# Optimization experiments

Measured on AMD Instinct MI355X. Metric: run time of the kernel, lower is better.

Reference implementation:

```python
import jax, jax.numpy as jnp
import numpy as np

N = 50000   # total nodes (50 graphs x 1000 nodes)
E = 800000  # edges (avg degree 16)
H = 128     # hidden_dim == input_dim
B = 50      # number of graphs
L = 3       # n_GNN_layers
NEG = 0.2   # LeakyReLU slope
EPS = 1e-5  # BatchNorm eps


def _lrelu(v):
    return jnp.where(v >= 0, v, NEG * v)


def setup_inputs() -> dict:
    key = jax.random.key(0)
    ks = jax.random.split(key, 16)
    s = 0.05
    inp = {
        "x": jax.random.normal(ks[0], (N, H), jnp.float32),
        "edge_index": jax.random.randint(ks[1], (2, E), 0, N, dtype=jnp.int64),
        "edge_attr": jax.random.uniform(ks[2], (E,), jnp.float32),
        "batch": jnp.sort(jax.random.randint(ks[3], (N,), 0, B, dtype=jnp.int64)),
        # per-layer GCN params (3 identical-shape layers stacked on axis 0)
        "Wg": (jax.random.normal(ks[4], (L, H, H)) * s).astype(jnp.float32),   # GCNConv.lin (no bias)
        "bg": jnp.zeros((L, H), jnp.float32),                                  # GCNConv.bias
        "We": (jax.random.normal(ks[5], (L, 2 * H, H)) * s).astype(jnp.float32),  # edge_lin
        "be": jnp.zeros((L, H), jnp.float32),
        "Wl": (jax.random.normal(ks[6], (L, H, H)) * s).astype(jnp.float32),   # post-conv Linear
        "bl": jnp.zeros((L, H), jnp.float32),
        "gamma": jnp.ones((L, H), jnp.float32),                                # BatchNorm affine
        "beta": jnp.zeros((L, H), jnp.float32),
        # final MLP head
        "Wf1": (jax.random.normal(ks[7], (H, H)) * s).astype(jnp.float32),
        "bf1": jnp.zeros((H,), jnp.float32),
        "Wf2": (jax.random.normal(ks[8], (H, H // 2)) * s).astype(jnp.float32),
        "bf2": jnp.zeros((H // 2,), jnp.float32),
        "Wf3": (jax.random.normal(ks[9], (H // 2, 2)) * s).astype(jnp.float32),
        "bf3": jnp.zeros((2,), jnp.float32),
    }
    return inp


def reference(x, edge_index, edge_attr, batch, Wg, bg, We, be, Wl, bl, gamma, beta,
              Wf1, bf1, Wf2, bf2, Wf3, bf3):
    n = x.shape[0]
    # edge_attr = |edge_attr| is used only for gcn_norm's edge weights, which the
    # 'node_concate' message ignores; self-loops from gcn_norm DO affect messages.
    _ = jnp.abs(edge_attr)
    loop = jnp.arange(n, dtype=edge_index.dtype)
    row = jnp.concatenate([edge_index[0], loop])  # source j
    col = jnp.concatenate([edge_index[1], loop])  # target i

    z = x
    for l in range(L):
        h = z @ Wg[l]                                           # GCNConv.lin (bias=False)
        msg = jnp.concatenate([h[col], h[row]], axis=1) @ We[l] + be[l]  # edge_lin(cat[x_i, x_j])
        agg = jax.ops.segment_sum(msg, col, num_segments=n) + bg[l]      # scatter-add + conv bias
        h2 = _lrelu(agg @ Wl[l] + bl[l])                        # Linear + LeakyReLU(0.2)
        mu = h2.mean(axis=0)
        var = h2.var(axis=0)                                    # biased var (BatchNorm training)
        z = gamma[l] * (h2 - mu) * jax.lax.rsqrt(var + EPS) + beta[l]

    # global_mean_pool over graph segments
    sums = jax.ops.segment_sum(z, batch, num_segments=B)
    cnt = jax.ops.segment_sum(jnp.ones((n, 1), z.dtype), batch, num_segments=B)
    pooled = sums / jnp.maximum(cnt, 1.0)

    h = _lrelu(pooled @ Wf1 + bf1)
    h = _lrelu(h @ Wf2 + bf2)
    return h @ Wf3 + bf3
```

## Files before the change

### kernel.cpp

```cpp
#include <hip/hip_runtime.h>
#include <hip/hip_fp16.h>

#define H 128
#define NEG 0.2f
#define EPSBN 1e-5f
#define BM 32

__device__ __forceinline__ float lrelu(float v){ return v >= 0.f ? v : NEG*v; }

union HU { __half2 h; unsigned int u; };

typedef __attribute__((ext_vector_type(8))) short bf16x8;
typedef __attribute__((ext_vector_type(4))) float f32x4;
#define MFMA16(a,b,c) __builtin_amdgcn_mfma_f32_16x16x32_bf16(a,b,c,0,0,0)

__device__ __forceinline__ unsigned short bf16_rn(float x){
  unsigned int u = __float_as_uint(x);
  u += 0x7fffu + ((u >> 16) & 1u);
  return (unsigned short)(u >> 16);
}
__device__ __forceinline__ float bf16f(unsigned short h){
  return __uint_as_float(((unsigned int)h) << 16);
}

__global__ void prep1_kernel(const float* __restrict__ We, const float* __restrict__ Wl,
                             float* __restrict__ Ntmp){
  int l = blockIdx.x >> 7;
  int k = blockIdx.x & 127;
  int j = threadIdx.x;
  __shared__ float WeS[2*H];
  if (j < H) WeS[j] = We[(size_t)(l*2*H + k)*H + j];
  else       WeS[j] = We[(size_t)(l*2*H + 128 + k)*H + (j-128)];
  __syncthreads();
  const float* wl = Wl + (size_t)l*H*H;
  int sel = (j >> 7) << 7;
  int jj = j & 127;
  float acc = 0.f;
  #pragma unroll 8
  for (int m=0;m<H;m++) acc += WeS[sel + m] * wl[m*H + jj];
  Ntmp[(size_t)(l*H + k)*256 + j] = acc;
}

__global__ void prep2_kernel(const float* __restrict__ Wg, const float* __restrict__ Ntmp,
                             float* __restrict__ Mcomb){
  int l = blockIdx.x >> 7;
  int k = blockIdx.x & 127;
  int j = threadIdx.x;
  __shared__ float WgS[H];
  if (j < H) WgS[j] = Wg[(size_t)(l*H + k)*H + j];
  __syncthreads();
  const float* nt = Ntmp + (size_t)l*H*256;
  float acc = 0.f;
  #pragma unroll 8
  for (int m=0;m<H;m++) acc += WgS[m] * nt[m*256 + j];
  Mcomb[(size_t)(l*H + k)*256 + j] = acc;
}

__global__ void prep3_kernel(const float* __restrict__ Mcomb,
                             unsigned short* __restrict__ Mfh, unsigned short* __restrict__ Mfl){
  int bid = blockIdx.x;
  int l  = bid >> 6;
  int ks = (bid >> 4) & 3;
  int ct = bid & 15;
  int lane = threadIdx.x;
  const float* M = Mcomb + (size_t)l*H*256;
  size_t base = ((((size_t)l*4 + ks)*16 + ct)*64 + lane)*8;
  int col = ct*16 + (lane & 15);
  int g = lane >> 4;
  #pragma unroll
  for (int j=0;j<8;j++){
    int k = ks*32 + 8*g + j;
    float v = M[(size_t)k*256 + col];
    unsigned short hi = bf16_rn(v);
    unsigned short lo = bf16_rn(v - bf16f(hi));
    Mfh[base + j] = hi;
    Mfl[base + j] = lo;
  }
}

__global__ void prepc_kernel(const float* __restrict__ be, const float* __restrict__ bg,
                             const float* __restrict__ bl, const float* __restrict__ Wl,
                             float* __restrict__ c1c2){
  int l = blockIdx.x;
  int j = threadIdx.x;
  const float* wl = Wl + (size_t)l*H*H;
  float a1=0.f, a2=0.f;
  for (int m=0;m<H;m++){ float w = wl[m*H + j]; a1 += be[l*H+m]*w; a2 += bg[l*H+m]*w; }
  c1c2[l*2*H + j]     = a1;
  c1c2[l*2*H + H + j] = a2 + bl[l*H + j];
}

__global__ void deg_kernel(const int* __restrict__ ei, int E, int* __restrict__ degI,
                           unsigned short* __restrict__ rankA){
  int e = blockIdx.x*blockDim.x + threadIdx.x;
  if (e < E){
    int r = atomicAdd(&degI[ei[E + e]], 1);
    rankA[e] = (unsigned short)r;
  }
}

__global__ void scan1_kernel(const int* __restrict__ degI, int n,
                             int* __restrict__ incl, int* __restrict__ bsum){
  int i = blockIdx.x*256 + threadIdx.x;
  __shared__ int sh[256];
  int v = (i < n) ? degI[i] : 0;
  sh[threadIdx.x] = v;
  __syncthreads();
  for (int ofs=1; ofs<256; ofs<<=1){
    int t = (threadIdx.x >= ofs) ? sh[threadIdx.x - ofs] : 0;
    __syncthreads();
    sh[threadIdx.x] += t;
    __syncthreads();
  }
  if (i < n) incl[i] = sh[threadIdx.x];
  if (threadIdx.x == 255) bsum[blockIdx.x] = sh[255];
}

__global__ void scan2_kernel(int* __restrict__ bsum, int nb){
  __shared__ int sh[256];
  int v = (threadIdx.x < nb) ? bsum[threadIdx.x] : 0;
  sh[threadIdx.x] = v;
  __syncthreads();
  for (int ofs=1; ofs<256; ofs<<=1){
    int t = (threadIdx.x >= ofs) ? sh[threadIdx.x - ofs] : 0;
    __syncthreads();
    sh[threadIdx.x] += t;
    __syncthreads();
  }
  if (threadIdx.x < nb) bsum[threadIdx.x] = sh[threadIdx.x] - v;
}

__global__ void scan3_kernel(const int* __restrict__ incl, const int* __restrict__ degI,
                             const int* __restrict__ bexcl, int n, int E,
                             int* __restrict__ rowptr){
  int i = blockIdx.x*256 + threadIdx.x;
  if (i < n){
    int start = incl[i] - degI[i] + bexcl[blockIdx.x];
    rowptr[i] = start;
    if (i == n-1) rowptr[n] = E;
  }
}

__global__ void fill_kernel(const int* __restrict__ ei, int E,
                            const int* __restrict__ rowptr, const unsigned short* __restrict__ rankA,
                            unsigned short* __restrict__ csr_src){
  int e = blockIdx.x*256 + threadIdx.x;
  if (e < E){
    int c = ei[E + e];
    int pos = rowptr[c] + (int)rankA[e];
    csr_src[pos] = (unsigned short)ei[e];
  }
}

__global__ void gofs_kernel(const int* __restrict__ batch, int n, int B, int* __restrict__ gofs){
  int i = blockIdx.x*256 + threadIdx.x;
  if (i >= n) return;
  if (i == 0){
    int b0 = batch[0];
    for (int g=0; g<=b0; g++) gofs[g] = 0;
  } else {
    int bp = batch[i-1], bc = batch[i];
    for (int g=bp+1; g<=bc; g++) gofs[g] = i;
  }
  if (i == n-1){
    int bl = batch[n-1];
    for (int g=bl+1; g<=B; g++) gofs[g] = n;
  }
}

template<int XF>
__global__ __launch_bounds__(256)
void gemm_kernel(const float* __restrict__ Zin, const float* __restrict__ bnp,
                 const unsigned short* __restrict__ Mfh, const unsigned short* __restrict__ Mfl,
                 const float* __restrict__ c1c2, const int* __restrict__ degI,
                 int n, float* __restrict__ pre, __half* __restrict__ Vh){
  __shared__ float As[32*132];
  int brow = blockIdx.x * BM;
  int t = threadIdx.x;

  {
    int srow = t >> 3, sf = t & 7;
    int gr = brow + srow;
    bool act = (gr < n);
    const float* zrow = Zin + (size_t)gr*H;
    #pragma unroll
    for (int u=0; u<4; u++){
      int c4 = sf + 8*u;
      float4 g = make_float4(0.f,0.f,0.f,0.f);
      if (act) g = *reinterpret_cast<const float4*>(&zrow[c4*4]);
      if (XF){
        float4 sc4 = *reinterpret_cast<const float4*>(&bnp[c4*4]);
        float4 sh4 = *reinterpret_cast<const float4*>(&bnp[H + c4*4]);
        g.x = lrelu(g.x)*sc4.x + sh4.x;
        g.y = lrelu(g.y)*sc4.y + sh4.y;
        g.z = lrelu(g.z)*sc4.z + sh4.z;
        g.w = lrelu(g.w)*sc4.w + sh4.w;
      }
      *reinterpret_cast<float4*>(&As[srow*132 + c4*4]) = g;
    }
  }
  __syncthreads();

  int lane = t & 63;
  int w = t >> 6;
  int rowtile = w & 1, colgroup = w >> 1;

  f32x4 accU[4], accV[4];
  #pragma unroll
  for (int i=0;i<4;i++){
    accU[i] = (f32x4){0.f,0.f,0.f,0.f};
    accV[i] = (f32x4){0.f,0.f,0.f,0.f};
  }

  const bf16x8* Bh = reinterpret_cast<const bf16x8*>(Mfh);
  const bf16x8* Bl = reinterpret_cast<const bf16x8*>(Mfl);
  int arow_ = rowtile*16 + (lane & 15);
  int agrp  = (lane >> 4) << 3;

  #pragma unroll 1
  for (int ks=0; ks<4; ks++){
    int aofs = arow_*132 + ks*32 + agrp;
    float av[8];
    *reinterpret_cast<float4*>(&av[0]) = *reinterpret_cast<const float4*>(&As[aofs]);
    *reinterpret_cast<float4*>(&av[4]) = *reinterpret_cast<const float4*>(&As[aofs + 4]);
    bf16x8 ah, al;
    #pragma unroll
    for (int j=0;j<8;j++){
      unsigned short h = bf16_rn(av[j]);
      ah[j] = (short)h;
      al[j] = (short)bf16_rn(av[j] - bf16f(h));
    }
    #pragma unroll
    for (int ctu=0; ctu<4; ctu++){
      int ctU = colgroup*4 + ctu;
      int ctV = ctU + 8;
      bf16x8 bhU = Bh[(ks*16 + ctU)*64 + lane];
      bf16x8 blU = Bl[(ks*16 + ctU)*64 + lane];
      bf16x8 bhV = Bh[(ks*16 + ctV)*64 + lane];
      accU[ctu] = MFMA16(ah, bhU, accU[ctu]);
      accU[ctu] = MFMA16(al, bhU, accU[ctu]);
      accU[ctu] = MFMA16(ah, blU, accU[ctu]);
      accV[ctu] = MFMA16(ah, bhV, accV[ctu]);
      accV[ctu] = MFMA16(al, bhV, accV[ctu]);
    }
  }

  int rowbase = brow + rowtile*16 + ((lane >> 4) << 2);
  float dg[4];
  #pragma unroll
  for (int r=0;r<4;r++){
    int gr = rowbase + r;
    dg[r] = (gr < n) ? (float)(degI[gr] + 1) : 0.f;
  }
  #pragma unroll
  for (int ctu=0; ctu<4; ctu++){
    int colU = colgroup*64 + ctu*16 + (lane & 15);
    float c1v = c1c2[colU], c2v = c1c2[H + colU];
    #pragma unroll
    for (int r=0;r<4;r++){
      int gr = rowbase + r;
      if (gr < n){
        float uu = accU[ctu][r], vv = accV[ctu][r];
        pre[(size_t)gr*H + colU] = dg[r]*(uu + c1v) + c2v + vv;
        Vh [(size_t)gr*H + colU] = __float2half(vv);
      }
    }
  }
}

__global__ __launch_bounds__(256)
void agg_kernel(const int* __restrict__ rowptr, const unsigned short* __restrict__ csr_src,
                const __half* __restrict__ Vh, float* __restrict__ pre, int n,
                float* __restrict__ partial){
  int node = blockIdx.x*8 + (threadIdx.x >> 5);
  int lane = threadIdx.x & 31;
  float4 h4 = make_float4(0.f,0.f,0.f,0.f);
  float4 q4 = make_float4(0.f,0.f,0.f,0.f);
  if (node < n){
    int p  = rowptr[node];
    int pe = rowptr[node+1];
    const __half* Vb = Vh + lane*4;
    float4 a = make_float4(0.f,0.f,0.f,0.f);
    for (; p+8 <= pe; p+=8){
      int s0 = csr_src[p],   s1 = csr_src[p+1], s2 = csr_src[p+2], s3 = csr_src[p+3];
      int s4 = csr_src[p+4], s5 = csr_src[p+5], s6 = csr_src[p+6], s7 = csr_src[p+7];
      uint2 r0 = *reinterpret_cast<const uint2*>(&Vb[(size_t)s0*H]);
      uint2 r1 = *reinterpret_cast<const uint2*>(&Vb[(size_t)s1*H]);
      uint2 r2 = *reinterpret_cast<const uint2*>(&Vb[(size_t)s2*H]);
      uint2 r3 = *reinterpret_cast<const uint2*>(&Vb[(size_t)s3*H]);
      uint2 r4 = *reinterpret_cast<const uint2*>(&Vb[(size_t)s4*H]);
      uint2 r5 = *reinterpret_cast<const uint2*>(&Vb[(size_t)s5*H]);
      uint2 r6 = *reinterpret_cast<const uint2*>(&Vb[(size_t)s6*H]);
      uint2 r7 = *reinterpret_cast<const uint2*>(&Vb[(size_t)s7*H]);
      HU ua, ub;
      float2 fa, fb;
      ua.u=r0.x; ub.u=r0.y; fa=__half22float2(ua.h); fb=__half22float2(ub.h);
      a.x+=fa.x; a.y+=fa.y; a.z+=fb.x; a.w+=fb.y;
      ua.u=r1.x; ub.u=r1.y; fa=__half22float2(ua.h); fb=__half22float2(ub.h);
      a.x+=fa.x; a.y+=fa.y; a.z+=fb.x; a.w+=fb.y;
      ua.u=r2.x; ub.u=r2.y; fa=__half22float2(ua.h); fb=__half22float2(ub.h);
      a.x+=fa.x; a.y+=fa.y; a.z+=fb.x; a.w+=fb.y;
      ua.u=r3.x; ub.u=r3.y; fa=__half22float2(ua.h); fb=__half22float2(ub.h);
      a.x+=fa.x; a.y+=fa.y; a.z+=fb.x; a.w+=fb.y;
      ua.u=r4.x; ub.u=r4.y; fa=__half22float2(ua.h); fb=__half22float2(ub.h);
      a.x+=fa.x; a.y+=fa.y; a.z+=fb.x; a.w+=fb.y;
      ua.u=r5.x; ub.u=r5.y; fa=__half22float2(ua.h); fb=__half22float2(ub.h);
      a.x+=fa.x; a.y+=fa.y; a.z+=fb.x; a.w+=fb.y;
      ua.u=r6.x; ub.u=r6.y; fa=__half22float2(ua.h); fb=__half22float2(ub.h);
      a.x+=fa.x; a.y+=fa.y; a.z+=fb.x; a.w+=fb.y;
      ua.u=r7.x; ub.u=r7.y; fa=__half22float2(ua.h); fb=__half22float2(ub.h);
      a.x+=fa.x; a.y+=fa.y; a.z+=fb.x; a.w+=fb.y;
    }
    for (; p+2 <= pe; p+=2){
      int s0 = csr_src[p], s1 = csr_src[p+1];
      uint2 r0 = *reinterpret_cast<const uint2*>(&Vb[(size_t)s0*H]);
      uint2 r1 = *reinterpret_cast<const uint2*>(&Vb[(size_t)s1*H]);
      HU ua, ub;
      float2 fa, fb;
      ua.u=r0.x; ub.u=r0.y; fa=__half22float2(ua.h); fb=__half22float2(ub.h);
      a.x+=fa.x; a.y+=fa.y; a.z+=fb.x; a.w+=fb.y;
      ua.u=r1.x; ub.u=r1.y; fa=__half22float2(ua.h); fb=__half22float2(ub.h);
      a.x+=fa.x; a.y+=fa.y; a.z+=fb.x; a.w+=fb.y;
    }
    for (; p < pe; p++){
      int s = csr_src[p];
      uint2 r = *reinterpret_cast<const uint2*>(&Vb[(size_t)s*H]);
      HU ua, ub; ua.u = r.x; ub.u = r.y;
      float2 fa = __half22float2(ua.h), fb = __half22float2(ub.h);
      a.x += fa.x; a.y += fa.y; a.z += fb.x; a.w += fb.y;
    }
    float4* pp = reinterpret_cast<float4*>(&pre[(size_t)node*H + lane*4]);
    float4 pr = *pp;
    pr.x += a.x; pr.y += a.y; pr.z += a.z; pr.w += a.w;
    *pp = pr;
    h4.x = lrelu(pr.x); h4.y = lrelu(pr.y); h4.z = lrelu(pr.z); h4.w = lrelu(pr.w);
    q4.x = h4.x*h4.x;   q4.y = h4.y*h4.y;   q4.z = h4.z*h4.z;   q4.w = h4.w*h4.w;
  }
  __shared__ float4 red[8][32];
  int slot = threadIdx.x >> 5;
  red[slot][lane] = h4;
  __syncthreads();
  if (threadIdx.x < 32){
    float4 tt = red[0][threadIdx.x];
    #pragma unroll
    for (int r=1;r<8;r++){
      float4 v = red[r][threadIdx.x];
      tt.x += v.x; tt.y += v.y; tt.z += v.z; tt.w += v.w;
    }
    *reinterpret_cast<float4*>(&partial[(size_t)blockIdx.x*256 + threadIdx.x*4]) = tt;
  }
  __syncthreads();
  red[slot][lane] = q4;
  __syncthreads();
  if (threadIdx.x < 32){
    float4 tt = red[0][threadIdx.x];
    #pragma unroll
    for (int r=1;r<8;r++){
      float4 v = red[r][threadIdx.x];
      tt.x += v.x; tt.y += v.y; tt.z += v.z; tt.w += v.w;
    }
    *reinterpret_cast<float4*>(&partial[(size_t)blockIdx.x*256 + 128 + threadIdx.x*4]) = tt;
  }
}

__global__ __launch_bounds__(256)
void redstats_kernel(const float* __restrict__ partial, int nb, float* __restrict__ bnsum,
                     const float* __restrict__ gamma, const float* __restrict__ beta,
                     float inv_n, float* __restrict__ scsh, int* __restrict__ cnt){
  int c = threadIdx.x;
  float acc = 0.f;
  for (int b = blockIdx.x; b < nb; b += 64)
    acc += partial[(size_t)b*256 + c];
  atomicAdd(&bnsum[c], acc);
  __threadfence();
  __shared__ int lastS;
  __syncthreads();
  if (threadIdx.x == 0){
    int prev = atomicAdd(cnt, 1);
    lastS = (prev == 63) ? 1 : 0;
  }
  __syncthreads();
  if (lastS && c < H){
    float s  = atomicAdd(&bnsum[c], 0.f);
    float ss = atomicAdd(&bnsum[H + c], 0.f);
    float mu  = s * inv_n;
    float var = ss * inv_n - mu*mu;
    float rs  = rsqrtf(fmaxf(var, 0.f) + EPSBN);
    float sc  = gamma[c] * rs;
    scsh[c]     = sc;
    scsh[H + c] = beta[c] - mu*sc;
  }
}

__global__ __launch_bounds__(256)
void pool_kernel(const float* __restrict__ pre, const float* __restrict__ scsh,
                 const int* __restrict__ gofs, float* __restrict__ pooled){
  int g    = blockIdx.x >> 3;
  int part = blockIdx.x & 7;
  int col  = threadIdx.x & 127;
  int half = threadIdx.x >> 7;
  int s = gofs[g], e = gofs[g+1];
  float sc = scsh[col], sh = scsh[H + col];
  float acc = 0.f;
  for (int r = s + part*2 + half; r < e; r += 16)
    acc += lrelu(pre[(size_t)r*H + col])*sc + sh;
  if (acc != 0.f || part == 0)
    atomicAdd(&pooled[(size_t)g*H + col], acc);
}

__global__ __launch_bounds__(128)
void head_kernel(const float* __restrict__ pooled, const int* __restrict__ gofs,
                 const float* __restrict__ Wf1, const float* __restrict__ bf1,
                 const float* __restrict__ Wf2, const float* __restrict__ bf2,
                 const float* __restrict__ Wf3, const float* __restrict__ bf3,
                 float* __restrict__ out){
  int g = blockIdx.x;
  int c = threadIdx.x;
  __shared__ float pm[128], h1[128], h2[64];
  float cf = fmaxf((float)(gofs[g+1] - gofs[g]), 1.f);
  pm[c] = pooled[(size_t)g*H + c] / cf;
  __syncthreads();
  float a = bf1[c];
  for (int k=0;k<H;k++) a += pm[k]*Wf1[k*H + c];
  h1[c] = lrelu(a);
  __syncthreads();
  if (c < 64){
    float b = bf2[c];
    for (int k=0;k<H;k++) b += h1[k]*Wf2[k*64 + c];
    h2[c] = lrelu(b);
  }
  __syncthreads();
  if (c < 2){
    float o = bf3[c];
    for (int k=0;k<64;k++) o += h2[k]*Wf3[k*2 + c];
    out[g*2 + c] = o;
  }
}

extern "C" void kernel_launch(void* const* d_in, const int* in_sizes, int n_in,
                              void* d_out, int out_size, void* d_ws, size_t ws_size,
                              hipStream_t stream){
  const float* x     = (const float*)d_in[0];
  const int*   ei    = (const int*)d_in[1];
  const int*   batch = (const int*)d_in[3];
  const float* Wg    = (const float*)d_in[4];
  const float* bg    = (const float*)d_in[5];
  const float* We    = (const float*)d_in[6];
  const float* be    = (const float*)d_in[7];
  const float* Wl    = (const float*)d_in[8];
  const float* bl    = (const float*)d_in[9];
  const float* gamma = (const float*)d_in[10];
  const float* beta  = (const float*)d_in[11];
  const float* Wf1   = (const float*)d_in[12];
  const float* bf1   = (const float*)d_in[13];
  const float* Wf2   = (const float*)d_in[14];
  const float* bf2   = (const float*)d_in[15];
  const float* Wf3   = (const float*)d_in[16];
  const float* bf3   = (const float*)d_in[17];
  float* out = (float*)d_out;

  int n = in_sizes[0] / H;
  int E = in_sizes[1] / 2;
  int B = out_size / 2;

  int nagg = (n + 7)/8;

  char* ws = (char*)d_ws;
  size_t off = 0;
  auto alloc = [&](size_t bytes)->void*{ void* p = ws + off; off += (bytes + 255) & ~255ULL; return p; };
  float*  pre    = (float*)alloc((size_t)n*H*4);
  __half* Vh     = (__half*)alloc((size_t)n*H*2);
  float*  Mcomb  = (float*)alloc((size_t)3*H*256*4);
  float*  Ntmp   = (float*)alloc((size_t)3*H*256*4);
  unsigned short* Mfh = (unsigned short*)alloc((size_t)3*4*16*64*8*2);
  unsigned short* Mfl = (unsigned short*)alloc((size_t)3*4*16*64*8*2);
  float*  c1c2   = (float*)alloc(3*2*H*4);
  float*  scsh   = (float*)alloc(3*2*H*4);
  int*    incl   = (int*)alloc((size_t)n*4);
  int*    bsum   = (int*)alloc(256*4);
  int*    rowptr = (int*)alloc((size_t)(n+1)*4);
  unsigned short* rankA   = (unsigned short*)alloc((size_t)E*2);
  unsigned short* csr_src = (unsigned short*)alloc((size_t)E*2);
  int*    gofs   = (int*)alloc((size_t)(B+1)*4);
  float*  partial= (float*)alloc((size_t)nagg*256*4);
  char* zbase = ws + off;
  float* bnsum  = (float*)alloc(3*2*H*4);
  int*   cnt    = (int*)alloc(3*4);
  int*   degI   = (int*)alloc((size_t)n*4);
  float* pooled = (float*)alloc((size_t)B*H*4);
  size_t zbytes = (size_t)((ws + off) - zbase);
  hipMemsetAsync(zbase, 0, zbytes, stream);

  prep1_kernel<<<3*H, 256, 0, stream>>>(We, Wl, Ntmp);
  prep2_kernel<<<3*H, 256, 0, stream>>>(Wg, Ntmp, Mcomb);
  prep3_kernel<<<3*64, 64, 0, stream>>>(Mcomb, Mfh, Mfl);
  prepc_kernel<<<3, 128, 0, stream>>>(be, bg, bl, Wl, c1c2);
  deg_kernel<<<(E+255)/256, 256, 0, stream>>>(ei, E, degI, rankA);

  int nb = (n + 255)/256;
  scan1_kernel<<<nb, 256, 0, stream>>>(degI, n, incl, bsum);
  scan2_kernel<<<1, 256, 0, stream>>>(bsum, nb);
  scan3_kernel<<<nb, 256, 0, stream>>>(incl, degI, bsum, n, E, rowptr);
  fill_kernel<<<(E+255)/256, 256, 0, stream>>>(ei, E, rowptr, rankA, csr_src);
  gofs_kernel<<<nb, 256, 0, stream>>>(batch, n, B, gofs);

  int gblocks = (n + BM - 1)/BM;
  size_t mstride = (size_t)4*16*64*8;
  for (int l=0; l<3; l++){
    if (l == 0)
      gemm_kernel<0><<<gblocks, 256, 0, stream>>>(x, nullptr, Mfh, Mfl, c1c2, degI, n, pre, Vh);
    else
      gemm_kernel<1><<<gblocks, 256, 0, stream>>>(pre, scsh + (l-1)*2*H, Mfh + l*mstride, Mfl + l*mstride,
                                                  c1c2 + l*2*H, degI, n, pre, Vh);
    agg_kernel<<<nagg, 256, 0, stream>>>(rowptr, csr_src, Vh, pre, n, partial);
    redstats_kernel<<<64, 256, 0, stream>>>(partial, nagg, bnsum + l*2*H,
                                            gamma + l*H, beta + l*H, 1.f/(float)n,
                                            scsh + l*2*H, cnt + l);
  }
  pool_kernel<<<B*8, 256, 0, stream>>>(pre, scsh + 2*2*H, gofs, pooled);
  head_kernel<<<B, 128, 0, stream>>>(pooled, gofs, Wf1, bf1, Wf2, bf2, Wf3, bf3, out);
}
```

Measured before the change: 406.8 us.

## Prefetch GEMM weight fragments into registers and fuse pooling into head kernel

The GEMM k-loop is fully unrolled with register double-buffering, so the weight fragments for the next k-step load while the current MFMAs run, and the first fragments are fetched before the shared-memory staging. Separately, the pool kernel is folded into the head kernel. Each of 50 blocks now sums its graph's rows itself and applies the BN affine algebraically (sc*sum + sh*count), which removes a launch and the atomics. The cost is higher register pressure in the GEMM and less parallelism for pooling (50 blocks instead of 400).

```diff
diff --git a/kernel.cpp b/kernel.cpp
--- a/kernel.cpp
+++ b/kernel.cpp
@@ -21,6 +21,18 @@
 }
 __device__ __forceinline__ float bf16f(unsigned short h){
   return __uint_as_float(((unsigned int)h) << 16);
+}
+
+__device__ __forceinline__ void asplit(const float* As, int aofs, bf16x8& ah, bf16x8& al){
+  float av[8];
+  *reinterpret_cast<float4*>(&av[0]) = *reinterpret_cast<const float4*>(&As[aofs]);
+  *reinterpret_cast<float4*>(&av[4]) = *reinterpret_cast<const float4*>(&As[aofs+4]);
+  #pragma unroll
+  for (int j=0;j<8;j++){
+    unsigned short h = bf16_rn(av[j]);
+    ah[j] = (short)h;
+    al[j] = (short)bf16_rn(av[j] - bf16f(h));
+  }
 }
 
 __global__ void prep1_kernel(const float* __restrict__ We, const float* __restrict__ Wl,
@@ -168,6 +180,21 @@
   }
 }
 
+#define KSBODY(KS, C, N, PREF) \
+  { bf16x8 ah, al; asplit(As, arow_*132 + (KS)*32 + agrp, ah, al); \
+    if (PREF){ int nb = fb + ((KS)+1)*1024; \
+      N##U0h = Bh[nb];     N##U1h = Bh[nb+64];  N##U2h = Bh[nb+128]; N##U3h = Bh[nb+192]; \
+      N##U0l = Bl[nb];     N##U1l = Bl[nb+64];  N##U2l = Bl[nb+128]; N##U3l = Bl[nb+192]; \
+      N##V0h = Bh[nb+512]; N##V1h = Bh[nb+576]; N##V2h = Bh[nb+640]; N##V3h = Bh[nb+704]; } \
+    accU[0]=MFMA16(ah,C##U0h,accU[0]); accU[0]=MFMA16(al,C##U0h,accU[0]); accU[0]=MFMA16(ah,C##U0l,accU[0]); \
+    accV[0]=MFMA16(ah,C##V0h,accV[0]); accV[0]=MFMA16(al,C##V0h,accV[0]); \
+    accU[1]=MFMA16(ah,C##U1h,accU[1]); accU[1]=MFMA16(al,C##U1h,accU[1]); accU[1]=MFMA16(ah,C##U1l,accU[1]); \
+    accV[1]=MFMA16(ah,C##V1h,accV[1]); accV[1]=MFMA16(al,C##V1h,accV[1]); \
+    accU[2]=MFMA16(ah,C##U2h,accU[2]); accU[2]=MFMA16(al,C##U2h,accU[2]); accU[2]=MFMA16(ah,C##U2l,accU[2]); \
+    accV[2]=MFMA16(ah,C##V2h,accV[2]); accV[2]=MFMA16(al,C##V2h,accV[2]); \
+    accU[3]=MFMA16(ah,C##U3h,accU[3]); accU[3]=MFMA16(al,C##U3h,accU[3]); accU[3]=MFMA16(ah,C##U3l,accU[3]); \
+    accV[3]=MFMA16(ah,C##V3h,accV[3]); accV[3]=MFMA16(al,C##V3h,accV[3]); }
+
 template<int XF>
 __global__ __launch_bounds__(256)
 void gemm_kernel(const float* __restrict__ Zin, const float* __restrict__ bnp,
@@ -177,6 +204,19 @@
   __shared__ float As[32*132];
   int brow = blockIdx.x * BM;
   int t = threadIdx.x;
+
+  int lane = t & 63;
+  int w = t >> 6;
+  int rowtile = w & 1, colgroup = w >> 1;
+  const bf16x8* Bh = reinterpret_cast<const bf16x8*>(Mfh);
+  const bf16x8* Bl = reinterpret_cast<const bf16x8*>(Mfl);
+  int fb = colgroup*4*64 + lane;
+
+  bf16x8 cU0h,cU1h,cU2h,cU3h, cU0l,cU1l,cU2l,cU3l, cV0h,cV1h,cV2h,cV3h;
+  bf16x8 nU0h,nU1h,nU2h,nU3h, nU0l,nU1l,nU2l,nU3l, nV0h,nV1h,nV2h,nV3h;
+  cU0h = Bh[fb];     cU1h = Bh[fb+64];  cU2h = Bh[fb+128]; cU3h = Bh[fb+192];
+  cU0l = Bl[fb];     cU1l = Bl[fb+64];  cU2l = Bl[fb+128]; cU3l = Bl[fb+192];
+  cV0h = Bh[fb+512]; cV1h = Bh[fb+576]; cV2h = Bh[fb+640]; cV3h = Bh[fb+704];
 
   {
     int srow = t >> 3, sf = t & 7;
@@ -201,49 +241,19 @@
   }
   __syncthreads();
 
-  int lane = t & 63;
-  int w = t >> 6;
-  int rowtile = w & 1, colgroup = w >> 1;
-
   f32x4 accU[4], accV[4];
   #pragma unroll
   for (int i=0;i<4;i++){
     accU[i] = (f32x4){0.f,0.f,0.f,0.f};
     accV[i] = (f32x4){0.f,0.f,0.f,0.f};
   }
-
-  const bf16x8* Bh = reinterpret_cast<const bf16x8*>(Mfh);
-  const bf16x8* Bl = reinterpret_cast<const bf16x8*>(Mfl);
   int arow_ = rowtile*16 + (lane & 15);
   int agrp  = (lane >> 4) << 3;
 
-  #pragma unroll 1
-  for (int ks=0; ks<4; ks++){
-    int aofs = arow_*132 + ks*32 + agrp;
-    float av[8];
-    *reinterpret_cast<float4*>(&av[0]) = *reinterpret_cast<const float4*>(&As[aofs]);
-    *reinterpret_cast<float4*>(&av[4]) = *reinterpret_cast<const float4*>(&As[aofs + 4]);
-    bf16x8 ah, al;
-    #pragma unroll
-    for (int j=0;j<8;j++){
-      unsigned short h = bf16_rn(av[j]);
-      ah[j] = (short)h;
-      al[j] = (short)bf16_rn(av[j] - bf16f(h));
-    }
-    #pragma unroll
-    for (int ctu=0; ctu<4; ctu++){
-      int ctU = colgroup*4 + ctu;
-      int ctV = ctU + 8;
-      bf16x8 bhU = Bh[(ks*16 + ctU)*64 + lane];
-      bf16x8 blU = Bl[(ks*16 + ctU)*64 + lane];
-      bf16x8 bhV = Bh[(ks*16 + ctV)*64 + lane];
-      accU[ctu] = MFMA16(ah, bhU, accU[ctu]);
-      accU[ctu] = MFMA16(al, bhU, accU[ctu]);
-      accU[ctu] = MFMA16(ah, blU, accU[ctu]);
-      accV[ctu] = MFMA16(ah, bhV, accV[ctu]);
-      accV[ctu] = MFMA16(al, bhV, accV[ctu]);
-    }
-  }
+  KSBODY(0, c, n, 1)
+  KSBODY(1, n, c, 1)
+  KSBODY(2, c, n, 1)
+  KSBODY(3, n, c, 0)
 
   int rowbase = brow + rowtile*16 + ((lane >> 4) << 2);
   float dg[4];
@@ -393,47 +403,46 @@
 }
 
 __global__ __launch_bounds__(256)
-void pool_kernel(const float* __restrict__ pre, const float* __restrict__ scsh,
-                 const int* __restrict__ gofs, float* __restrict__ pooled){
-  int g    = blockIdx.x >> 3;
-  int part = blockIdx.x & 7;
-  int col  = threadIdx.x & 127;
-  int half = threadIdx.x >> 7;
-  int s = gofs[g], e = gofs[g+1];
-  float sc = scsh[col], sh = scsh[H + col];
-  float acc = 0.f;
-  for (int r = s + part*2 + half; r < e; r += 16)
-    acc += lrelu(pre[(size_t)r*H + col])*sc + sh;
-  if (acc != 0.f || part == 0)
-    atomicAdd(&pooled[(size_t)g*H + col], acc);
-}
-
-__global__ __launch_bounds__(128)
-void head_kernel(const float* __restrict__ pooled, const int* __restrict__ gofs,
+void head_kernel(const float* __restrict__ pre, const float* __restrict__ scsh,
+                 const int* __restrict__ gofs,
                  const float* __restrict__ Wf1, const float* __restrict__ bf1,
                  const float* __restrict__ Wf2, const float* __restrict__ bf2,
                  const float* __restrict__ Wf3, const float* __restrict__ bf3,
                  float* __restrict__ out){
   int g = blockIdx.x;
-  int c = threadIdx.x;
+  int t = threadIdx.x;
+  int col = t & 127, half = t >> 7;
+  int s = gofs[g], e = gofs[g+1];
+  float acc = 0.f;
+  for (int r = s + half; r < e; r += 2)
+    acc += lrelu(pre[(size_t)r*H + col]);
+  __shared__ float ps[2][128];
   __shared__ float pm[128], h1[128], h2[64];
-  float cf = fmaxf((float)(gofs[g+1] - gofs[g]), 1.f);
-  pm[c] = pooled[(size_t)g*H + c] / cf;
-  __syncthreads();
-  float a = bf1[c];
-  for (int k=0;k<H;k++) a += pm[k]*Wf1[k*H + c];
-  h1[c] = lrelu(a);
-  __syncthreads();
-  if (c < 64){
-    float b = bf2[c];
-    for (int k=0;k<H;k++) b += h1[k]*Wf2[k*64 + c];
-    h2[c] = lrelu(b);
-  }
-  __syncthreads();
-  if (c < 2){
-    float o = bf3[c];
-    for (int k=0;k<64;k++) o += h2[k]*Wf3[k*2 + c];
-    out[g*2 + c] = o;
+  ps[half][col] = acc;
+  __syncthreads();
+  if (t < 128){
+    float cntf = (float)(e - s);
+    float cf = fmaxf(cntf, 1.f);
+    float sum = ps[0][t] + ps[1][t];
+    pm[t] = (scsh[t]*sum + scsh[H + t]*cntf) / cf;
+  }
+  __syncthreads();
+  if (t < 128){
+    float a = bf1[t];
+    for (int k=0;k<H;k++) a += pm[k]*Wf1[k*H + t];
+    h1[t] = lrelu(a);
+  }
+  __syncthreads();
+  if (t < 64){
+    float b = bf2[t];
+    for (int k=0;k<H;k++) b += h1[k]*Wf2[k*64 + t];
+    h2[t] = lrelu(b);
+  }
+  __syncthreads();
+  if (t < 2){
+    float o = bf3[t];
+    for (int k=0;k<64;k++) o += h2[k]*Wf3[k*2 + t];
+    out[g*2 + t] = o;
   }
 }
 
@@ -487,7 +496,6 @@
   float* bnsum  = (float*)alloc(3*2*H*4);
   int*   cnt    = (int*)alloc(3*4);
   int*   degI   = (int*)alloc((size_t)n*4);
-  float* pooled = (float*)alloc((size_t)B*H*4);
   size_t zbytes = (size_t)((ws + off) - zbase);
   hipMemsetAsync(zbase, 0, zbytes, stream);
 
@@ -517,6 +525,5 @@
                                             gamma + l*H, beta + l*H, 1.f/(float)n,
                                             scsh + l*2*H, cnt + l);
   }
-  pool_kernel<<<B*8, 256, 0, stream>>>(pre, scsh + 2*2*H, gofs, pooled);
-  head_kernel<<<B, 128, 0, stream>>>(pooled, gofs, Wf1, bf1, Wf2, bf2, Wf3, bf3, out);
-}
+  head_kernel<<<B, 256, 0, stream>>>(pre, scsh + 2*2*H, gofs, Wf1, bf1, Wf2, bf2, Wf3, bf3, out);
+}
```

After: 513.3 us. +26.2%, slower.
